# Kernel tuning notes

Hardware: AMD Instinct MI355X
Metric: run time of the kernel (lower is better)

Reference implementation:

```python
import jax, jax.numpy as jnp
import numpy as np

B, S, E = 2, 2048, 2048
H, KV, D = 32, 8, 128
EPS = 1e-6


def _rope_tables(seq_len, head_dim, base=1_000_000.0):
    inv_freq = 1.0 / (base ** (np.arange(0, head_dim, 2, dtype=np.float32) / head_dim))
    ang = np.arange(seq_len, dtype=np.float32)[:, None] * inv_freq[None, :]  # [S, D/2]
    cos = np.concatenate([np.cos(ang), np.cos(ang)], axis=-1)  # [S, D]
    sin = np.concatenate([np.sin(ang), np.sin(ang)], axis=-1)
    return jnp.asarray(cos), jnp.asarray(sin)


def setup_inputs() -> dict:
    key = jax.random.key(0)
    ks = jax.random.split(key, 8)
    x = jax.random.normal(ks[0], (B, S, E), dtype=jnp.float32)
    mask = jnp.triu(jnp.ones((S, S), dtype=bool), k=1)  # True = masked (causal)
    cos, sin = _rope_tables(S, D)
    w = 0.02
    Wq = jax.random.normal(ks[1], (E, H * D), dtype=jnp.float32) * w
    bq = jnp.zeros((H * D,), dtype=jnp.float32)
    Wk = jax.random.normal(ks[2], (E, KV * D), dtype=jnp.float32) * w
    bk = jnp.zeros((KV * D,), dtype=jnp.float32)
    Wv = jax.random.normal(ks[3], (E, KV * D), dtype=jnp.float32) * w
    bv = jnp.zeros((KV * D,), dtype=jnp.float32)
    Wo = jax.random.normal(ks[4], (H * D, E), dtype=jnp.float32) * w
    q_scale = jnp.ones((D,), dtype=jnp.float32)
    k_scale = jnp.ones((D,), dtype=jnp.float32)
    return {"x": x, "mask": mask, "cos": cos, "sin": sin, "Wq": Wq, "bq": bq,
            "Wk": Wk, "bk": bk, "Wv": Wv, "bv": bv, "Wo": Wo,
            "q_scale": q_scale, "k_scale": k_scale}


def _rmsnorm(x, scale):
    xf = x.astype(jnp.float32)
    var = jnp.mean(xf * xf, axis=-1, keepdims=True)
    return (xf * jax.lax.rsqrt(var + EPS) * scale).astype(x.dtype)


def _apply_rope(x, cos, sin):
    # x: [B, h, S, D]; cos/sin: [S, D]
    d2 = x.shape[-1] // 2
    x1, x2 = x[..., :d2], x[..., d2:]
    rotated = jnp.concatenate([-x2, x1], axis=-1)
    return (x * cos[None, None] + rotated * sin[None, None]).astype(x.dtype)


def reference(x, mask, cos, sin, Wq, bq, Wk, bk, Wv, bv, Wo, q_scale, k_scale):
    b, s, _ = x.shape
    q = (x @ Wq + bq).reshape(b, s, H, D).transpose(0, 2, 1, 3)   # [B,H,S,D]
    k = (x @ Wk + bk).reshape(b, s, KV, D).transpose(0, 2, 1, 3)  # [B,KV,S,D]
    v = (x @ Wv + bv).reshape(b, s, KV, D).transpose(0, 2, 1, 3)
    q = _rmsnorm(q, q_scale)
    k = _rmsnorm(k, k_scale)
    q = _apply_rope(q, cos, sin)
    k = _apply_rope(k, cos, sin)
    group = H // KV
    k = jnp.repeat(k, group, axis=1)  # repeat_interleave on head dim -> [B,H,S,D]
    v = jnp.repeat(v, group, axis=1)
    scores = jnp.einsum("bhqd,bhkd->bhqk", q, k)
    scores = jnp.where(mask[None, None], -jnp.inf, scores)
    attn = jax.nn.softmax(scores / jnp.sqrt(jnp.float32(D)), axis=-1)
    ctx = jnp.einsum("bhqk,bhkd->bhqd", attn, v)
    ctx = ctx.transpose(0, 2, 1, 3).reshape(b, s, H * D)
    return ctx @ Wo
```

## Files before the change

### kernel.cpp

```cpp
#include <hip/hip_runtime.h>

typedef short short8 __attribute__((ext_vector_type(8)));
typedef float f32x4 __attribute__((ext_vector_type(4)));
typedef float f32x16 __attribute__((ext_vector_type(16)));
typedef unsigned int uint2v __attribute__((ext_vector_type(2)));

static __device__ __forceinline__ ushort f2bf(float f){
  union { float f; uint u; } cv; cv.f = f;
  uint u = cv.u;
  uint r = (u + 0x7fffu + ((u >> 16) & 1u)) >> 16;
  return (ushort)r;
}
static __device__ __forceinline__ float bf2f(ushort h){
  union { uint u; float f; } cv; cv.u = ((uint)h) << 16; return cv.f;
}
static __device__ __forceinline__ f32x16 mfma32(short8 a, short8 b, f32x16 c){
  return __builtin_amdgcn_mfma_f32_32x32x16_bf16(a, b, c, 0, 0, 0);
}
static __device__ __forceinline__ float ex2(float x){
  float r; asm("v_exp_f32 %0, %1" : "=v"(r) : "v"(x)); return r;
}
static __device__ __forceinline__ uint cvtpk(float lo, float hi){
  uint r; asm("v_cvt_pk_bf16_f32 %0, %1, %2" : "=v"(r) : "v"(lo), "v"(hi)); return r;
}
static __device__ __forceinline__ void glds16(const void* g, const void* l){
  __builtin_amdgcn_global_load_lds((const __attribute__((address_space(1))) void*)g,
                                   (__attribute__((address_space(3))) void*)l, 16, 0, 0);
}
static __device__ __forceinline__ void store_out(float* p, float v){ *p = v; }
static __device__ __forceinline__ void store_out(ushort* p, float v){ *p = f2bf(v); }
static __device__ __forceinline__ int xcd_swizzle(int flat, int nwg){
  int q = nwg >> 3, r = nwg & 7;
  int xcd = flat & 7, idx = flat >> 3;
  return (xcd < r) ? xcd * (q + 1) + idx : r * (q + 1) + (xcd - r) * q + idx;
}

__global__ void cvt_bf16_kernel(const float* __restrict__ x, ushort* __restrict__ y, int n4){
  int i = blockIdx.x * 256 + threadIdx.x;
  if (i < n4){
    float4 v = reinterpret_cast<const float4*>(x)[i];
    ushort4 o; o.x = f2bf(v.x); o.y = f2bf(v.y); o.z = f2bf(v.z); o.w = f2bf(v.w);
    reinterpret_cast<ushort4*>(y)[i] = o;
  }
}

__global__ void addk_kernel(const float* __restrict__ p0, const float* __restrict__ p1,
                            float* __restrict__ out, int n4){
  int i = blockIdx.x * 256 + threadIdx.x;
  if (i < n4){
    float4 a = reinterpret_cast<const float4*>(p0)[i];
    float4 b = reinterpret_cast<const float4*>(p1)[i];
    float4 o; o.x = a.x + b.x; o.y = a.y + b.y; o.z = a.z + b.z; o.w = a.w + b.w;
    reinterpret_cast<float4*>(out)[i] = o;
  }
}

__global__ void transpose_cvt_kernel(const float* __restrict__ W, ushort* __restrict__ WT, int K, int N){
  __shared__ float tile[32][33];
  int n0 = blockIdx.x * 32, k0 = blockIdx.y * 32;
  int tx = threadIdx.x, ty = threadIdx.y;
  #pragma unroll
  for (int i = 0; i < 4; i++){ int r = ty + i * 8; tile[r][tx] = W[(size_t)(k0 + r) * N + n0 + tx]; }
  __syncthreads();
  #pragma unroll
  for (int i = 0; i < 4; i++){ int r = ty + i * 8; WT[(size_t)(n0 + r) * K + k0 + tx] = f2bf(tile[tx][r]); }
}

__global__ void bias_concat_kernel(const float* __restrict__ bq, const float* __restrict__ bk,
                                   const float* __restrict__ bv, float* __restrict__ out){
  int i = blockIdx.x * 256 + threadIdx.x;
  if (i < 6144) out[i] = (i < 4096) ? bq[i] : ((i < 5120) ? bk[i - 4096] : bv[i - 5120]);
}

template<typename OutT>
__global__ __launch_bounds__(512, 1) void gemm8p_kernel(const ushort* __restrict__ A, const ushort* __restrict__ BT,
                                                        const float* __restrict__ bias, OutT* __restrict__ C,
                                                        int M, int N, int K, int klen){
  __shared__ __align__(16) ushort As[2][2][128 * 64];
  __shared__ __align__(16) ushort Bs[2][2][128 * 64];
  const int nbx = N >> 8;
  const int nwg = nbx * (M >> 8);
  const int wg = xcd_swizzle(blockIdx.x, nwg);
  const int m0 = (wg / nbx) * 256, n0 = (wg % nbx) * 256;
  const int kb = blockIdx.y * klen;
  OutT* Cp = C + (size_t)blockIdx.y * M * N;
  const int tid = threadIdx.x, w = tid >> 6, l = tid & 63;
  const int l31 = l & 31, hi = l >> 5, swz = l31 & 7;
  const int wr = w >> 2, wc = w & 3;
  const int bhalf = wc >> 1, brow0 = (wc & 1) * 64;
  const int srow = tid >> 3, schunk = tid & 7;
  const int sg = schunk ^ (srow & 7);
  const int nt = klen >> 6;

#define STG(MAT, H, T, BUF) do{                                                            \
    const ushort* _s = (MAT) ? BT : A;                                                     \
    const int _rb = ((MAT) ? n0 : m0) + (H) * 128;                                         \
    ushort* _d = (MAT) ? &Bs[BUF][H][0] : &As[BUF][H][0];                                  \
    glds16(_s + (size_t)(_rb + srow) * K + kb + (size_t)(T) * 64 + sg * 8,                 \
           _d + (w * 64) * 8);                                                             \
    glds16(_s + (size_t)(_rb + 64 + srow) * K + kb + (size_t)(T) * 64 + sg * 8,            \
           _d + (512 + w * 64) * 8);                                                       \
  }while(0)

#define RD_AF(BUF, MTB) do{                                                                \
    _Pragma("unroll")                                                                      \
    for (int mt2 = 0; mt2 < 2; mt2++)                                                      \
      _Pragma("unroll")                                                                    \
      for (int ks = 0; ks < 4; ks++)                                                       \
        afr[mt2][ks] = *(const short8*)&As[BUF][wr]                                        \
            [(((MTB) + mt2) * 32 + l31) * 64 + (((ks * 2 + hi) ^ swz) * 8)];               \
  }while(0)

#define RD_BF(DST, BUF, NT) do{                                                            \
    _Pragma("unroll")                                                                      \
    for (int ks = 0; ks < 4; ks++)                                                         \
      DST[ks] = *(const short8*)&Bs[BUF][bhalf]                                            \
          [(brow0 + (NT) * 32 + l31) * 64 + (((ks * 2 + hi) ^ swz) * 8)];                  \
  }while(0)

#define MM(MTB, NT, BF) do{                                                                \
    __builtin_amdgcn_s_setprio(1);                                                        \
    _Pragma("unroll")                                                                      \
    for (int mt2 = 0; mt2 < 2; mt2++)                                                      \
      _Pragma("unroll")                                                                    \
      for (int ks = 0; ks < 4; ks++)                                                       \
        acc[(MTB) + mt2][NT] = mfma32(afr[mt2][ks], BF[ks], acc[(MTB) + mt2][NT]);         \
    __builtin_amdgcn_s_setprio(0);                                                        \
  }while(0)

  f32x16 acc[4][2] = {};
  short8 afr[2][4], bfr0[4], bfr1[4];
  STG(0, 0, 0, 0); STG(1, 0, 0, 0); STG(0, 1, 0, 0); STG(1, 1, 0, 0);
  for (int t = 0; t < nt; t++){
    const int buf = t & 1, nb = buf ^ 1;
    const bool pf = (t + 1 < nt);
    if (pf){ STG(0, 0, t + 1, nb); asm volatile("s_waitcnt vmcnt(2)" ::: "memory"); }
    else   { asm volatile("s_waitcnt vmcnt(0)" ::: "memory"); }
    __builtin_amdgcn_s_barrier();
    RD_AF(buf, 0); RD_BF(bfr0, buf, 0);
    MM(0, 0, bfr0);
    __builtin_amdgcn_s_barrier();
    RD_BF(bfr1, buf, 1);
    if (pf) STG(1, 0, t + 1, nb);
    __builtin_amdgcn_s_barrier();
    MM(0, 1, bfr1);
    __builtin_amdgcn_s_barrier();
    RD_AF(buf, 2);
    if (pf) STG(0, 1, t + 1, nb);
    __builtin_amdgcn_s_barrier();
    MM(2, 1, bfr1);
    __builtin_amdgcn_s_barrier();
    if (pf) STG(1, 1, t + 1, nb);
    __builtin_amdgcn_s_barrier();
    MM(2, 0, bfr0);
    __builtin_amdgcn_s_barrier();
  }
#undef STG
#undef RD_AF
#undef RD_BF
#undef MM
  #pragma unroll
  for (int mt = 0; mt < 4; mt++)
    #pragma unroll
    for (int ntl = 0; ntl < 2; ntl++){
      int col = n0 + wc * 64 + ntl * 32 + l31;
      float bb = bias ? bias[col] : 0.0f;
      #pragma unroll
      for (int reg = 0; reg < 16; reg++){
        int row = m0 + wr * 128 + mt * 32 + (reg & 3) + 8 * (reg >> 2) + 4 * hi;
        store_out(&Cp[(size_t)row * N + col], acc[mt][ntl][reg] + bb);
      }
    }
}

#define QSCL2 0.12752016f
__global__ __launch_bounds__(256) void norm_rope_kernel(const ushort* __restrict__ qkv,
    const float* __restrict__ cosT, const float* __restrict__ sinT,
    const float* __restrict__ qs, const float* __restrict__ ksc,
    ushort* __restrict__ qo, ushort* __restrict__ ko, ushort* __restrict__ vto){
  int slot = blockIdx.x * 4 + (threadIdx.x >> 6);
  int lane = threadIdx.x & 63;
  int row = slot / 48, c = slot % 48;
  int b = row >> 11, s = row & 2047;
  size_t base = (size_t)row * 6144 + c * 128;
  float e1 = bf2f(qkv[base + lane]);
  float e2 = bf2f(qkv[base + lane + 64]);
  if (c < 40){
    float ss = e1 * e1 + e2 * e2;
    #pragma unroll
    for (int m = 1; m < 64; m <<= 1) ss += __shfl_xor(ss, m);
    float rs = rsqrtf(ss * (1.0f / 128.0f) + 1e-6f);
    const float* sc = (c < 32) ? qs : ksc;
    float n1 = e1 * rs * sc[lane], n2 = e2 * rs * sc[lane + 64];
    float c1 = cosT[s * 128 + lane],      s1 = sinT[s * 128 + lane];
    float c2 = cosT[s * 128 + lane + 64], s2 = sinT[s * 128 + lane + 64];
    float o1 = n1 * c1 - n2 * s1;
    float o2 = n2 * c2 + n1 * s2;
    if (c < 32){
      size_t ob = ((size_t)(b * 32 + c) * 2048 + s) * 128;
      qo[ob + lane] = f2bf(o1 * QSCL2); qo[ob + lane + 64] = f2bf(o2 * QSCL2);
    } else {
      int kv = c - 32;
      size_t ob = ((size_t)(b * 8 + kv) * 2048 + s) * 128;
      ko[ob + lane] = f2bf(o1); ko[ob + lane + 64] = f2bf(o2);
    }
  } else {
    int kv = c - 40;
    size_t ob = (size_t)(b * 8 + kv) * 128;
    vto[(ob + lane) * 2048 + s]      = f2bf(e1);
    vto[(ob + lane + 64) * 2048 + s] = f2bf(e2);
  }
}

__global__ __launch_bounds__(256, 2) void flash_kernel(const ushort* __restrict__ Q, const ushort* __restrict__ Kg,
    const ushort* __restrict__ VTg, ushort* __restrict__ ctx){
  __shared__ ushort Kl[2][64 * 128];
  __shared__ ushort Vl[2][128 * 64];
  const int bh = blockIdx.y, b = bh >> 5, h = bh & 31, kvh = h >> 2;
  const int bx = blockIdx.x;
  const int tid = threadIdx.x, w = tid >> 6, l = tid & 63;
  const int q31 = l & 31, hi = l >> 5, swz = q31 & 7;
  const ushort* Kbase = Kg  + (size_t)(b * 8 + kvh) * 2048 * 128;
  const ushort* Vbase = VTg + (size_t)(b * 8 + kvh) * 128 * 2048;
  const int krow = l >> 4, kcol = l & 15;
  const int vrow = l >> 3, vcol = l & 7;

  #define STAGE(KT, BS) do {                                                            \
    _Pragma("unroll")                                                                   \
    for (int i2 = 0; i2 < 4; i2++){                                                     \
      int i = w * 4 + i2; int row = i * 4 + krow;                                       \
      glds16(Kbase + (size_t)((KT) * 64 + row) * 128 + ((kcol ^ (row & 7)) * 8),        \
             &Kl[BS][i * 512]);                                                         \
    }                                                                                   \
    _Pragma("unroll")                                                                   \
    for (int j2 = 0; j2 < 4; j2++){                                                     \
      int j = w * 4 + j2; int row = j * 8 + vrow;                                       \
      glds16(Vbase + (size_t)row * 2048 + (KT) * 64 + ((vcol ^ (row & 7)) * 8),         \
             &Vl[BS][j * 512]);                                                         \
    }                                                                                   \
  } while (0)

  for (int pass = 0; pass < 2; pass++){
    const int qb = pass ? bx : (15 - bx);
    const int q0 = qb * 128;
    const int qw = q0 + w * 32;
    const int myq = qw + q31;
    const ushort* Qp = Q + ((size_t)(b * 32 + h) * 2048 + myq) * 128;
    short8 qf[8];
    #pragma unroll
    for (int s = 0; s < 8; s++) qf[s] = *(const short8*)(Qp + s * 16 + hi * 8);
    f32x16 o[4] = {};
    float m_r = -INFINITY, l_r = 0.f;
    const int nt = 2 * qb + 2;

    STAGE(0, 0);
    for (int kt = 0; kt < nt; kt++){
      const int cur = kt & 1;
      if (kt + 1 < nt){
        STAGE(kt + 1, cur ^ 1);
        asm volatile("s_waitcnt vmcnt(8)" ::: "memory");
      } else {
        asm volatile("s_waitcnt vmcnt(0)" ::: "memory");
      }
      __builtin_amdgcn_s_barrier();
      asm volatile("" ::: "memory");
      f32x16 sa0 = {}, sa1 = {};
      __builtin_amdgcn_s_setprio(1);
      #pragma unroll
      for (int s = 0; s < 8; s++){
        short8 a0 = *(const short8*)&Kl[cur][q31 * 128 + (((2 * s + hi) ^ swz) * 8)];
        short8 a1 = *(const short8*)&Kl[cur][(32 + q31) * 128 + (((2 * s + hi) ^ swz) * 8)];
        sa0 = mfma32(a0, qf[s], sa0);
        sa1 = mfma32(a1, qf[s], sa1);
      }
      __builtin_amdgcn_s_setprio(0);
      if (kt >= 2 * qb){
        #pragma unroll
        for (int r = 0; r < 16; r++){
          int krel = (r & 3) + 8 * (r >> 2) + 4 * hi;
          if (kt * 64 + krel > myq)      sa0[r] = -INFINITY;
          if (kt * 64 + 32 + krel > myq) sa1[r] = -INFINITY;
        }
      }
      float mx = fmaxf(sa0[0], sa1[0]);
      #pragma unroll
      for (int r = 1; r < 16; r++) mx = fmaxf(mx, fmaxf(sa0[r], sa1[r]));
      mx = fmaxf(mx, __shfl_xor(mx, 32));
      if (!__all(mx - m_r <= 8.f)){
        float mn = fmaxf(m_r, mx);
        float al = ex2(m_r - mn);
        m_r = mn; l_r *= al;
        #pragma unroll
        for (int r = 0; r < 16; r++){
          float alq = __shfl(al, (r & 3) + 8 * (r >> 2) + 4 * hi);
          o[0][r] *= alq; o[1][r] *= alq; o[2][r] *= alq; o[3][r] *= alq;
        }
      }
      float rsum = 0.f;
      #pragma unroll
      for (int r = 0; r < 16; r++){
        sa0[r] = ex2(sa0[r] - m_r);
        sa1[r] = ex2(sa1[r] - m_r);
        rsum += sa0[r] + sa1[r];
      }
      rsum += __shfl_xor(rsum, 32);
      l_r += rsum;
      uint pk0[8], pk1[8];
      #pragma unroll
      for (int t = 0; t < 8; t++){
        pk0[t] = cvtpk(sa0[2 * t], sa0[2 * t + 1]);
        pk1[t] = cvtpk(sa1[2 * t], sa1[2 * t + 1]);
      }
      __builtin_amdgcn_s_setprio(1);
      #pragma unroll
      for (int sub = 0; sub < 2; sub++){
        #pragma unroll
        for (int kc = 0; kc < 2; kc++){
          uint p0 = sub ? pk1[4 * kc]     : pk0[4 * kc];
          uint p1 = sub ? pk1[4 * kc + 1] : pk0[4 * kc + 1];
          uint p2 = sub ? pk1[4 * kc + 2] : pk0[4 * kc + 2];
          uint p3 = sub ? pk1[4 * kc + 3] : pk0[4 * kc + 3];
          uint2v r02 = __builtin_amdgcn_permlane32_swap(p0, p2, false, false);
          uint2v r13 = __builtin_amdgcn_permlane32_swap(p1, p3, false, false);
          union { uint u[4]; short8 v; } Af;
          Af.u[0] = r02[0]; Af.u[1] = r13[0]; Af.u[2] = r02[1]; Af.u[3] = r13[1];
          #pragma unroll
          for (int dc = 0; dc < 4; dc++){
            short8 vf = *(const short8*)&Vl[cur][(dc * 32 + q31) * 64 + (((4 * sub + 2 * kc + hi) ^ swz) * 8)];
            o[dc] = mfma32(Af.v, vf, o[dc]);
          }
        }
      }
      __builtin_amdgcn_s_setprio(0);
      asm volatile("" ::: "memory");
      __builtin_amdgcn_s_barrier();
    }
    float invl = 1.0f / l_r;
    ushort* Cp = ctx + (size_t)(b * 2048 + qw) * 4096 + (size_t)h * 128;
    #pragma unroll
    for (int r = 0; r < 16; r++){
      int qrel = (r & 3) + 8 * (r >> 2) + 4 * hi;
      float inv = __shfl(invl, qrel);
      #pragma unroll
      for (int dc = 0; dc < 4; dc++)
        Cp[(size_t)qrel * 4096 + dc * 32 + q31] = f2bf(o[dc][r] * inv);
    }
  }
  #undef STAGE
}

extern "C" void kernel_launch(void* const* d_in, const int* in_sizes, int n_in,
                              void* d_out, int out_size, void* d_ws, size_t ws_size,
                              hipStream_t stream){
  const float* x    = (const float*)d_in[0];
  const float* cosT = (const float*)d_in[2];
  const float* sinT = (const float*)d_in[3];
  const float* Wq   = (const float*)d_in[4];
  const float* bq   = (const float*)d_in[5];
  const float* Wk   = (const float*)d_in[6];
  const float* bk   = (const float*)d_in[7];
  const float* Wv   = (const float*)d_in[8];
  const float* bv   = (const float*)d_in[9];
  const float* Wo   = (const float*)d_in[10];
  const float* qs   = (const float*)d_in[11];
  const float* ksc  = (const float*)d_in[12];
  float* out = (float*)d_out;
  char* ws = (char*)d_ws;

  ushort* xb    = (ushort*)(ws + 0);
  ushort* wtqkv = (ushort*)(ws + 16777216);
  float*  biasq = (float* )(ws + 41943040);
  ushort* qkv   = (ushort*)(ws + 41967616);
  ushort* qb_   = (ushort*)(ws + 92299264);
  ushort* kb_   = (ushort*)(ws + 125853696);
  ushort* vtb   = (ushort*)(ws + 134242304);
  ushort* ctx   = (ushort*)(ws + 142630912);
  ushort* wot   = (ushort*)(ws + 176185344);
  float* part   = (float*)(ws + 41967616);

  cvt_bf16_kernel<<<8192, 256, 0, stream>>>(x, xb, 2097152);
  transpose_cvt_kernel<<<dim3(128, 64), dim3(32, 8), 0, stream>>>(Wq, wtqkv, 2048, 4096);
  transpose_cvt_kernel<<<dim3(32, 64),  dim3(32, 8), 0, stream>>>(Wk, wtqkv + (size_t)4096 * 2048, 2048, 1024);
  transpose_cvt_kernel<<<dim3(32, 64),  dim3(32, 8), 0, stream>>>(Wv, wtqkv + (size_t)5120 * 2048, 2048, 1024);
  transpose_cvt_kernel<<<dim3(64, 128), dim3(32, 8), 0, stream>>>(Wo, wot, 4096, 2048);
  bias_concat_kernel<<<24, 256, 0, stream>>>(bq, bk, bv, biasq);

  gemm8p_kernel<ushort><<<dim3(384, 1), 512, 0, stream>>>(xb, wtqkv, biasq, qkv, 4096, 6144, 2048, 2048);
  norm_rope_kernel<<<49152, 256, 0, stream>>>(qkv, cosT, sinT, qs, ksc, qb_, kb_, vtb);
  flash_kernel<<<dim3(8, 64), 256, 0, stream>>>(qb_, kb_, vtb, ctx);
  gemm8p_kernel<float><<<dim3(128, 2), 512, 0, stream>>>(ctx, wot, nullptr, part, 4096, 2048, 4096, 2048);
  addk_kernel<<<8192, 256, 0, stream>>>(part, part + (size_t)4096 * 2048, out, 2097152);
}
```

Measured before the change: 417.3 us.

## Switch GEMM to 16x16x32 MFMA tiles and unroll double-buffer loop by two

The 8-wave GEMM now uses 16x16x32 bf16 MFMA instead of 32x32x16, so the per-wave fragment layout, LDS read indexing, swizzle and epilogue store mapping are all reworked. The K loop is manually unrolled by two so the buffer indices become compile-time constants, and the LDS destination addressing in the staging macro is simplified to tid-based offsets. The aim is better LDS-read and MFMA interleaving and fewer runtime index computations. The cost is more accumulator registers and smaller MFMAs, which issue more instructions for the same work. The unrolled loop also assumes the K tile count per split is even.

```diff
diff --git a/kernel.cpp b/kernel.cpp
--- a/kernel.cpp
+++ b/kernel.cpp
@@ -13,6 +13,9 @@
 }
 static __device__ __forceinline__ float bf2f(ushort h){
   union { uint u; float f; } cv; cv.u = ((uint)h) << 16; return cv.f;
+}
+static __device__ __forceinline__ f32x4 mfma16(short8 a, short8 b, f32x4 c){
+  return __builtin_amdgcn_mfma_f32_16x16x32_bf16(a, b, c, 0, 0, 0);
 }
 static __device__ __forceinline__ f32x16 mfma32(short8 a, short8 b, f32x16 c){
   return __builtin_amdgcn_mfma_f32_32x32x16_bf16(a, b, c, 0, 0, 0);
@@ -84,91 +87,108 @@
   const int m0 = (wg / nbx) * 256, n0 = (wg % nbx) * 256;
   const int kb = blockIdx.y * klen;
   OutT* Cp = C + (size_t)blockIdx.y * M * N;
-  const int tid = threadIdx.x, w = tid >> 6, l = tid & 63;
-  const int l31 = l & 31, hi = l >> 5, swz = l31 & 7;
+  const int tid = threadIdx.x, w = tid >> 6, l = tid & 63, lm = l & 15, lk = l >> 4;
   const int wr = w >> 2, wc = w & 3;
-  const int bhalf = wc >> 1, brow0 = (wc & 1) * 64;
-  const int srow = tid >> 3, schunk = tid & 7;
-  const int sg = schunk ^ (srow & 7);
-  const int nt = klen >> 6;
+  const int bh = wc >> 1, brow = (wc & 1) * 64;
+  const int sw = lm & 7;
+  const int srow = tid >> 3, sch = tid & 7;
+  const int sg = sch ^ (srow & 7);
+  const int J = (klen >> 6) >> 1;
 
 #define STG(MAT, H, T, BUF) do{                                                            \
     const ushort* _s = (MAT) ? BT : A;                                                     \
     const int _rb = ((MAT) ? n0 : m0) + (H) * 128;                                         \
     ushort* _d = (MAT) ? &Bs[BUF][H][0] : &As[BUF][H][0];                                  \
     glds16(_s + (size_t)(_rb + srow) * K + kb + (size_t)(T) * 64 + sg * 8,                 \
-           _d + (w * 64) * 8);                                                             \
+           _d + tid * 8);                                                                  \
     glds16(_s + (size_t)(_rb + 64 + srow) * K + kb + (size_t)(T) * 64 + sg * 8,            \
-           _d + (512 + w * 64) * 8);                                                       \
+           _d + 4096 + tid * 8);                                                           \
   }while(0)
 
-#define RD_AF(BUF, MTB) do{                                                                \
+#define RD_AF(BUF, MH) do{                                                                 \
     _Pragma("unroll")                                                                      \
-    for (int mt2 = 0; mt2 < 2; mt2++)                                                      \
+    for (int mi = 0; mi < 4; mi++)                                                         \
       _Pragma("unroll")                                                                    \
-      for (int ks = 0; ks < 4; ks++)                                                       \
-        afr[mt2][ks] = *(const short8*)&As[BUF][wr]                                        \
-            [(((MTB) + mt2) * 32 + l31) * 64 + (((ks * 2 + hi) ^ swz) * 8)];               \
+      for (int ks = 0; ks < 2; ks++)                                                       \
+        af[mi][ks] = *(const short8*)&As[BUF][wr]                                          \
+            [((MH) * 64 + mi * 16 + lm) * 64 + (((ks * 4 + lk) ^ sw) * 8)];                \
   }while(0)
 
-#define RD_BF(DST, BUF, NT) do{                                                            \
+#define RD_BF(DST, BUF, NH) do{                                                            \
     _Pragma("unroll")                                                                      \
-    for (int ks = 0; ks < 4; ks++)                                                         \
-      DST[ks] = *(const short8*)&Bs[BUF][bhalf]                                            \
-          [(brow0 + (NT) * 32 + l31) * 64 + (((ks * 2 + hi) ^ swz) * 8)];                  \
+    for (int ni = 0; ni < 2; ni++)                                                         \
+      _Pragma("unroll")                                                                    \
+      for (int ks = 0; ks < 2; ks++)                                                       \
+        DST[ni][ks] = *(const short8*)&Bs[BUF][bh]                                         \
+            [(brow + (NH) * 32 + ni * 16 + lm) * 64 + (((ks * 4 + lk) ^ sw) * 8)];         \
   }while(0)
 
-#define MM(MTB, NT, BF) do{                                                                \
+#define MM(MH, NH, BF) do{                                                                 \
     __builtin_amdgcn_s_setprio(1);                                                        \
     _Pragma("unroll")                                                                      \
-    for (int mt2 = 0; mt2 < 2; mt2++)                                                      \
+    for (int mi = 0; mi < 4; mi++)                                                         \
       _Pragma("unroll")                                                                    \
-      for (int ks = 0; ks < 4; ks++)                                                       \
-        acc[(MTB) + mt2][NT] = mfma32(afr[mt2][ks], BF[ks], acc[(MTB) + mt2][NT]);         \
+      for (int ni = 0; ni < 2; ni++)                                                       \
+        _Pragma("unroll")                                                                  \
+        for (int ks = 0; ks < 2; ks++)                                                     \
+          acc[(MH)*4+mi][(NH)*2+ni] = mfma16(af[mi][ks], BF[ni][ks], acc[(MH)*4+mi][(NH)*2+ni]); \
     __builtin_amdgcn_s_setprio(0);                                                        \
   }while(0)
 
-  f32x16 acc[4][2] = {};
-  short8 afr[2][4], bfr0[4], bfr1[4];
+#define BAR() __builtin_amdgcn_s_barrier()
+#define FENCE() asm volatile("" ::: "memory")
+
+  f32x4 acc[8][4] = {};
+  short8 af[4][2], bf01[2][2], bf23[2][2];
   STG(0, 0, 0, 0); STG(1, 0, 0, 0); STG(0, 1, 0, 0); STG(1, 1, 0, 0);
-  for (int t = 0; t < nt; t++){
-    const int buf = t & 1, nb = buf ^ 1;
-    const bool pf = (t + 1 < nt);
-    if (pf){ STG(0, 0, t + 1, nb); asm volatile("s_waitcnt vmcnt(2)" ::: "memory"); }
-    else   { asm volatile("s_waitcnt vmcnt(0)" ::: "memory"); }
-    __builtin_amdgcn_s_barrier();
-    RD_AF(buf, 0); RD_BF(bfr0, buf, 0);
-    MM(0, 0, bfr0);
-    __builtin_amdgcn_s_barrier();
-    RD_BF(bfr1, buf, 1);
-    if (pf) STG(1, 0, t + 1, nb);
-    __builtin_amdgcn_s_barrier();
-    MM(0, 1, bfr1);
-    __builtin_amdgcn_s_barrier();
-    RD_AF(buf, 2);
-    if (pf) STG(0, 1, t + 1, nb);
-    __builtin_amdgcn_s_barrier();
-    MM(2, 1, bfr1);
-    __builtin_amdgcn_s_barrier();
-    if (pf) STG(1, 1, t + 1, nb);
-    __builtin_amdgcn_s_barrier();
-    MM(2, 0, bfr0);
-    __builtin_amdgcn_s_barrier();
+  for (int j = 0; j < J; j++){
+    const int t0 = 2 * j;
+    const bool lastit = (j == J - 1);
+    STG(0, 0, t0 + 1, 1);
+    asm volatile("s_waitcnt vmcnt(2)" ::: "memory");
+    BAR(); FENCE();
+    RD_AF(0, 0); RD_BF(bf01, 0, 0);
+    MM(0, 0, bf01);
+    BAR();
+    RD_BF(bf23, 0, 1);
+    STG(1, 0, t0 + 1, 1);
+    BAR(); MM(0, 1, bf23); BAR();
+    RD_AF(0, 1);
+    STG(0, 1, t0 + 1, 1);
+    BAR(); MM(1, 1, bf23); BAR();
+    STG(1, 1, t0 + 1, 1);
+    BAR(); MM(1, 0, bf01); BAR();
+    if (!lastit){ STG(0, 0, t0 + 2, 0); asm volatile("s_waitcnt vmcnt(2)" ::: "memory"); }
+    else        { asm volatile("s_waitcnt vmcnt(0)" ::: "memory"); }
+    BAR(); FENCE();
+    RD_AF(1, 0); RD_BF(bf01, 1, 0);
+    MM(0, 0, bf01);
+    BAR();
+    RD_BF(bf23, 1, 1);
+    if (!lastit) STG(1, 0, t0 + 2, 0);
+    BAR(); MM(0, 1, bf23); BAR();
+    RD_AF(1, 1);
+    if (!lastit) STG(0, 1, t0 + 2, 0);
+    BAR(); MM(1, 1, bf23); BAR();
+    if (!lastit) STG(1, 1, t0 + 2, 0);
+    BAR(); MM(1, 0, bf01); BAR();
   }
 #undef STG
 #undef RD_AF
 #undef RD_BF
 #undef MM
+#undef BAR
+#undef FENCE
   #pragma unroll
-  for (int mt = 0; mt < 4; mt++)
+  for (int mi = 0; mi < 8; mi++)
     #pragma unroll
-    for (int ntl = 0; ntl < 2; ntl++){
-      int col = n0 + wc * 64 + ntl * 32 + l31;
+    for (int ni = 0; ni < 4; ni++){
+      int col = n0 + wc * 64 + ni * 16 + lm;
       float bb = bias ? bias[col] : 0.0f;
       #pragma unroll
-      for (int reg = 0; reg < 16; reg++){
-        int row = m0 + wr * 128 + mt * 32 + (reg & 3) + 8 * (reg >> 2) + 4 * hi;
-        store_out(&Cp[(size_t)row * N + col], acc[mt][ntl][reg] + bb);
+      for (int r = 0; r < 4; r++){
+        int row = m0 + wr * 128 + mi * 16 + lk * 4 + r;
+        store_out(&Cp[(size_t)row * N + col], acc[mi][ni][r] + bb);
       }
     }
 }
```

After: 429.2 us. 2.9% more time.
